# Performance work log

Measured on AMD Instinct MI355X. Metric: run time of the kernel, lower is better.

The kernel has to match this reference:

```python
import jax, jax.numpy as jnp
import numpy as np

B, T, W, D = 2, 64, 32, 512
H = 8                      # n_heads
N = 64                     # d_state
EXPAND = 2
DIN = EXPAND * D           # 1024 d_inner
R = -(-D // 16)            # dt_rank = ceil(d_model/16) = 32
K = 4                      # d_conv (mamba default)


def setup_inputs():
    key = jax.random.key(0)
    ks = jax.random.split(key, 20)
    s = 0.02
    inp = {
        'x': jax.random.normal(ks[0], (B, T, W, D), jnp.float32),
        'wq': jax.random.normal(ks[1], (D, D), jnp.float32) * s,
        'bq': jnp.zeros((D,), jnp.float32),
        'wk': jax.random.normal(ks[2], (D, D), jnp.float32) * s,
        'bk': jnp.zeros((D,), jnp.float32),
        'wv': jax.random.normal(ks[3], (D, D), jnp.float32) * s,
        'bv': jnp.zeros((D,), jnp.float32),
        'wo': jax.random.normal(ks[4], (D, D), jnp.float32) * s,
        'bo': jnp.zeros((D,), jnp.float32),
        'in_proj_w': jax.random.normal(ks[5], (2 * DIN, D), jnp.float32) * s,
        'conv_w': jax.random.normal(ks[6], (DIN, 1, K), jnp.float32) * 0.2,
        'conv_b': jnp.zeros((DIN,), jnp.float32),
        'x_proj_w': jax.random.normal(ks[7], (R + 2 * N, DIN), jnp.float32) * s,
        'dt_proj_w': jax.random.normal(ks[8], (DIN, R), jnp.float32) * 0.1,
        'dt_proj_b': jnp.full((DIN,), -4.6, jnp.float32),  # ~softplus^-1(0.01)
        'A_log': jnp.log(jnp.broadcast_to(jnp.arange(1, N + 1, dtype=jnp.float32), (DIN, N))),
        'D_param': jnp.ones((DIN,), jnp.float32),
        'out_proj_w': jax.random.normal(ks[9], (D, DIN), jnp.float32) * s,
        'ln_w': jnp.ones((D,), jnp.float32),
        'ln_b': jnp.zeros((D,), jnp.float32),
    }
    return inp


def _attention(xf, wq, bq, wk, bk, wv, bv, wo, bo):
    b, L, d = xf.shape
    e = d // H
    q = (xf @ wq.T + bq).reshape(b, L, H, e)
    k = (xf @ wk.T + bk).reshape(b, L, H, e)
    v = (xf @ wv.T + bv).reshape(b, L, H, e)
    scale = 1.0 / jnp.sqrt(jnp.float32(e))
    scores = jnp.einsum('blhe,bshe->bhls', q, k) * scale
    causal = jnp.tril(jnp.ones((L, L), bool))
    scores = jnp.where(causal, scores, jnp.finfo(scores.dtype).min)
    attn = jax.nn.softmax(scores, axis=-1)  # dropout off (eval mode)
    out = jnp.einsum('bhls,bshe->blhe', attn, v).reshape(b, L, d)
    return out @ wo.T + bo


def _mamba(xf, in_proj_w, conv_w, conv_b, x_proj_w, dt_proj_w, dt_proj_b,
           A_log, D_param, out_proj_w):
    b, L, d = xf.shape
    xz = xf @ in_proj_w.T                 # (B,L,2*DIN)
    x_in, z = jnp.split(xz, 2, axis=-1)
    # causal depthwise conv1d over L
    xc = jnp.transpose(x_in, (0, 2, 1))   # (B,DIN,L)
    xc = jax.lax.conv_general_dilated(
        xc, conv_w, window_strides=(1,), padding=[(K - 1, 0)],
        feature_group_count=DIN, dimension_numbers=('NCH', 'OIH', 'NCH'))
    xc = xc + conv_b[None, :, None]
    u = jax.nn.silu(jnp.transpose(xc, (0, 2, 1)))   # (B,L,DIN)
    dbc = u @ x_proj_w.T                             # (B,L,R+2N)
    dt, Bm, Cm = dbc[..., :R], dbc[..., R:R + N], dbc[..., R + N:]
    dt = jax.nn.softplus(dt @ dt_proj_w.T + dt_proj_b)  # (B,L,DIN)
    A = -jnp.exp(A_log)                                 # (DIN,N)

    def step(h, t):
        dt_t, B_t, C_t, u_t = t  # (b,DIN),(b,N),(b,N),(b,DIN)
        dA = jnp.exp(dt_t[..., None] * A)                       # (b,DIN,N)
        h = dA * h + (dt_t * u_t)[..., None] * B_t[:, None, :]  # (b,DIN,N)
        y = jnp.einsum('bdn,bn->bd', h, C_t)
        return h, y

    h0 = jnp.zeros((b, DIN, N), xf.dtype)
    xs = (jnp.swapaxes(dt, 0, 1), jnp.swapaxes(Bm, 0, 1),
          jnp.swapaxes(Cm, 0, 1), jnp.swapaxes(u, 0, 1))
    _, ys = jax.lax.scan(step, h0, xs)
    y = jnp.swapaxes(ys, 0, 1) + u * D_param   # (B,L,DIN)
    y = y * jax.nn.silu(z)
    return y @ out_proj_w.T


def reference(x, wq, bq, wk, bk, wv, bv, wo, bo, in_proj_w, conv_w, conv_b,
              x_proj_w, dt_proj_w, dt_proj_b, A_log, D_param, out_proj_w,
              ln_w, ln_b):
    b, t, w, d = x.shape
    L = t * w
    xf = x.reshape(b, L, d)
    x_attn = _attention(xf, wq, bq, wk, bk, wv, bv, wo, bo).reshape(b, t, w, d)
    x_mamba = _mamba(xf, in_proj_w, conv_w, conv_b, x_proj_w, dt_proj_w,
                     dt_proj_b, A_log, D_param, out_proj_w).reshape(b, t, w, d)
    h = x + x_attn + x_mamba
    mu = jnp.mean(h, axis=-1, keepdims=True)
    var = jnp.mean(jnp.square(h - mu), axis=-1, keepdims=True)
    return (h - mu) * jax.lax.rsqrt(var + 1e-5) * ln_w + ln_b
```

## Files before the change

### kernel.cpp

```cpp
#include <hip/hip_runtime.h>

typedef __attribute__((ext_vector_type(4))) float f32x4;
typedef __attribute__((ext_vector_type(8))) short short8;
typedef __attribute__((ext_vector_type(2))) unsigned uint2e;

#define DEV static __device__ __forceinline__

DEV ushort f2b(float f) {
  union { float f; unsigned u; } v; v.f = f;
  unsigned r = v.u + 0x7FFF + ((v.u >> 16) & 1);
  return (ushort)(r >> 16);
}
DEV unsigned pack_bf2(float lo, float hi) {
  return (unsigned)f2b(lo) | ((unsigned)f2b(hi) << 16);
}
DEV float bflo(unsigned p) { return __uint_as_float(p << 16); }
DEV float bfhi(unsigned p) { return __uint_as_float(p & 0xFFFF0000u); }
DEV float b2f(ushort u) { return __uint_as_float((unsigned)u << 16); }

DEV float fexp2(float x) { float r; asm("v_exp_f32 %0, %1" : "=v"(r) : "v"(x)); return r; }

DEV float xor32_add_lo(float s) {
  uint2e r = __builtin_amdgcn_permlane32_swap(__float_as_uint(s), __float_as_uint(s), false, false);
  return s + __uint_as_float(r.x);
}

DEV void gl_lds16(const ushort* g, ushort* l) {
  __builtin_amdgcn_global_load_lds(
      (const __attribute__((address_space(1))) unsigned int*)g,
      (__attribute__((address_space(3))) unsigned int*)l, 16, 0, 0);
}

#define QP(x, ctrl) __int_as_float(__builtin_amdgcn_update_dpp(0, __float_as_int(x), (ctrl), 0xf, 0xf, false))
#define SWZ(x, off) __int_as_float(__builtin_amdgcn_ds_swizzle(__float_as_int(x), (off)))
#define DPP_ADD(x, ctrl, rmask) \
  ((x) + __int_as_float(__builtin_amdgcn_update_dpp(0, __float_as_int(x), (ctrl), (rmask), 0xf, false)))

#define LOG2E 1.44269504f

#define BB    2
#define LL    2048
#define DD    512
#define HH    8
#define EE    64
#define DIN   1024
#define NS    64
#define RR    32
#define BL    4096
#define NCH   16
#define TC    128
#define NC    1536
#define NQ    3584
#define XOFF  1536
#define ZOFF  2560
#define MFMA(a,b,c) __builtin_amdgcn_mfma_f32_16x16x32_bf16((a),(b),(c),0,0,0)

struct CvtJobs {
  const float* src[7];
  ushort*      dst[7];
  int          n[7];
};

__global__ __launch_bounds__(256) void cvt_multi(CvtJobs j) {
  int job = blockIdx.y;
  const float* s = j.src[job];
  ushort* d = j.dst[job];
  int n = j.n[job];
  for (int i = blockIdx.x * 256 + threadIdx.x; i < n; i += gridDim.x * 256)
    d[i] = f2b(s[i]);
}

__global__ __launch_bounds__(256) void pack_wcomb(
    const float* __restrict__ wo, const float* __restrict__ opw,
    const float* __restrict__ bq, const float* __restrict__ bk,
    const float* __restrict__ bv, ushort* __restrict__ wc,
    float* __restrict__ bqi)
{
  int i = blockIdx.x * 256 + threadIdx.x;
  if (i < NQ)
    bqi[i] = (i < DD) ? bq[i] : (i < 2 * DD) ? bk[i - DD] : (i < NC) ? bv[i - 2 * DD] : 0.f;
  if (i >= DD * NC) return;
  int n = i / NC, c = i - n * NC;
  float v = (c < DD) ? wo[n * DD + c] : opw[n * DIN + (c - DD)];
  wc[i] = f2b(v);
}

__global__ __launch_bounds__(256) void gemm_bt(
    const ushort* __restrict__ A, const ushort* __restrict__ W,
    const float* __restrict__ bias, float* __restrict__ outF,
    ushort* __restrict__ outB, int M, int N, int K, int act)
{
  __shared__ ushort As[64 * 32];
  __shared__ ushort Ws[64 * 32];
  int m0 = blockIdx.y * 64, n0 = blockIdx.x * 64;
  int tid = threadIdx.x, l = tid & 63, w = tid >> 6;
  int wm = (w >> 1) * 32, wn = (w & 1) * 32;
  int lr = l & 15, kl = (l >> 4) * 8;
  int srow = w * 16 + (l >> 2), scol = (l & 3) * 8;
  const ushort* gA = A + (size_t)(m0 + srow) * K + scol;
  const ushort* gW = W + (size_t)(n0 + srow) * K + scol;
  ushort* lA = As + w * 512;
  ushort* lW = Ws + w * 512;
  f32x4 acc[2][2] = {};

  for (int k0 = 0; k0 < K; k0 += 32) {
    __syncthreads();
    gl_lds16(gA, lA);
    gl_lds16(gW, lW);
    __syncthreads();
    short8 a0 = *(const short8*)&As[(wm + lr) * 32 + kl];
    short8 a1 = *(const short8*)&As[(wm + 16 + lr) * 32 + kl];
    short8 b0 = *(const short8*)&Ws[(wn + lr) * 32 + kl];
    short8 b1 = *(const short8*)&Ws[(wn + 16 + lr) * 32 + kl];
    acc[0][0] = MFMA(a0, b0, acc[0][0]);
    acc[0][1] = MFMA(a0, b1, acc[0][1]);
    acc[1][0] = MFMA(a1, b0, acc[1][0]);
    acc[1][1] = MFMA(a1, b1, acc[1][1]);
    gA += 32; gW += 32;
  }

  #pragma unroll
  for (int mi = 0; mi < 2; mi++)
    #pragma unroll
    for (int ni = 0; ni < 2; ni++) {
      int rbase = m0 + wm + mi * 16 + ((l >> 4) << 2);
      int col = n0 + wn + ni * 16 + lr;
      float bval = bias ? bias[col] : 0.f;
      #pragma unroll
      for (int r = 0; r < 4; r++) {
        float v = acc[mi][ni][r] + bval;
        if (act == 1) v = (v > 20.f) ? v : log1pf(__expf(v));
        size_t o = (size_t)(rbase + r) * N + col;
        if (outF) outF[o] = v;
        if (outB) outB[o] = f2b(v);
      }
    }
}

__global__ __launch_bounds__(256) void gemm128(
    const ushort* __restrict__ A, const ushort* __restrict__ W,
    const float* __restrict__ bias, float* __restrict__ outF,
    ushort* __restrict__ outB, int M, int N, int K)
{
  __shared__ ushort As[128 * 32];
  __shared__ ushort Ws[128 * 32];
  int tid = threadIdx.x, l = tid & 63, w = tid >> 6;
  int m0 = blockIdx.y * 128, n0 = blockIdx.x * 128;
  int wm = (w >> 1) * 64, wn = (w & 1) * 64;
  int lr = l & 15, kl = (l >> 4) * 8;
  f32x4 acc[4][4] = {};

  int srow = w * 32 + (l >> 2), scol = (l & 3) * 8;
  const ushort* gA0 = A + (size_t)(m0 + srow) * K + scol;
  const ushort* gA1 = gA0 + (size_t)16 * K;
  const ushort* gW0 = W + (size_t)(n0 + srow) * K + scol;
  const ushort* gW1 = gW0 + (size_t)16 * K;
  ushort* lA0 = As + w * 1024;
  ushort* lA1 = As + w * 1024 + 512;
  ushort* lW0 = Ws + w * 1024;
  ushort* lW1 = Ws + w * 1024 + 512;

  for (int k0 = 0; k0 < K; k0 += 32) {
    __syncthreads();
    gl_lds16(gA0, lA0);
    gl_lds16(gA1, lA1);
    gl_lds16(gW0, lW0);
    gl_lds16(gW1, lW1);
    __syncthreads();
    short8 af[4], bf[4];
    #pragma unroll
    for (int mi = 0; mi < 4; mi++) af[mi] = *(const short8*)&As[(wm + mi * 16 + lr) * 32 + kl];
    #pragma unroll
    for (int ni = 0; ni < 4; ni++) bf[ni] = *(const short8*)&Ws[(wn + ni * 16 + lr) * 32 + kl];
    #pragma unroll
    for (int mi = 0; mi < 4; mi++)
      #pragma unroll
      for (int ni = 0; ni < 4; ni++)
        acc[mi][ni] = MFMA(af[mi], bf[ni], acc[mi][ni]);
    gA0 += 32; gA1 += 32; gW0 += 32; gW1 += 32;
  }

  #pragma unroll
  for (int mi = 0; mi < 4; mi++)
    #pragma unroll
    for (int ni = 0; ni < 4; ni++) {
      int rbase = m0 + wm + mi * 16 + ((l >> 4) << 2);
      int col = n0 + wn + ni * 16 + lr;
      float bval = bias ? bias[col] : 0.f;
      #pragma unroll
      for (int r = 0; r < 4; r++) {
        float v = acc[mi][ni][r] + bval;
        size_t o = (size_t)(rbase + r) * N + col;
        if (outF) outF[o] = v;
        if (outB) outB[o] = f2b(v);
      }
    }
}

__global__ __launch_bounds__(256) void attn_xproj(
    const ushort* __restrict__ qkv, ushort* __restrict__ comb,
    const ushort* __restrict__ ub, const ushort* __restrict__ xpw,
    float* __restrict__ dbc)
{
  __shared__ ushort smem[4 * 64 * 72];
  int id = blockIdx.x;
  int tid = threadIdx.x, l = tid & 63, w = tid >> 6;

  if (id < 512) {
    typedef ushort row72[72];
    row72* Qs = (row72*)smem;
    row72* Ks = Qs + 64;
    row72* Vt = Ks + 64;
    row72* Ps = Vt + 64;
    int qt = 31 - (id & 31), h = (id >> 5) & 7, b = id >> 8;
    int w16 = w * 16, lr = l & 15, kl = (l >> 4) * 8;

    for (int i = tid; i < 512; i += 256) {
      int row = i >> 3, c8 = (i & 7) * 8;
      *(uint4*)&Qs[row][c8] =
          *(const uint4*)&qkv[((size_t)(b * LL + qt * 64 + row)) * NQ + h * EE + c8];
    }
    __syncthreads();

    float l_r[4] = {0.f, 0.f, 0.f, 0.f};
    f32x4 oacc[4] = {};
    const float SSC = 0.125f * LOG2E;

    for (int kv = 0; kv <= qt; kv++) {
      for (int i = tid; i < 512; i += 256) {
        int s = i >> 3, c8 = (i & 7) * 8;
        size_t rb = ((size_t)(b * LL + kv * 64 + s)) * NQ + h * EE + c8;
        *(uint4*)&Ks[s][c8] = *(const uint4*)&qkv[rb + DD];
        uint4 vv = *(const uint4*)&qkv[rb + 2 * DD];
        const ushort* pv = (const ushort*)&vv;
        #pragma unroll
        for (int jj = 0; jj < 8; jj++) Vt[c8 + jj][s] = pv[jj];
      }
      __syncthreads();

      f32x4 sacc[4] = {};
      #pragma unroll
      for (int kk = 0; kk < 2; kk++) {
        short8 aq = *(const short8*)&Qs[w16 + lr][kk * 32 + kl];
        #pragma unroll
        for (int nt = 0; nt < 4; nt++) {
          short8 bk8 = *(const short8*)&Ks[nt * 16 + lr][kk * 32 + kl];
          sacc[nt] = MFMA(aq, bk8, sacc[nt]);
        }
      }

      bool diag = (kv == qt);
      #pragma unroll
      for (int r = 0; r < 4; r++) {
        int rloc = w16 + ((l >> 4) << 2) + r;
        float rs = 0.f;
        #pragma unroll
        for (int nt = 0; nt < 4; nt++) {
          float v = sacc[nt][r] * SSC;
          if (diag && (nt * 16 + lr) > rloc) v = -1e30f;
          float p = fexp2(v);
          rs += p;
          Ps[rloc][nt * 16 + lr] = f2b(p);
        }
        rs += QP(rs, 0xB1);
        rs += QP(rs, 0x4E);
        rs += SWZ(rs, 0x101F);
        rs += SWZ(rs, 0x201F);
        l_r[r] += rs;
      }

      #pragma unroll
      for (int kk = 0; kk < 2; kk++) {
        short8 ap = *(const short8*)&Ps[w16 + lr][kk * 32 + kl];
        #pragma unroll
        for (int nt = 0; nt < 4; nt++) {
          short8 bv8 = *(const short8*)&Vt[nt * 16 + lr][kk * 32 + kl];
          oacc[nt] = MFMA(ap, bv8, oacc[nt]);
        }
      }
      __syncthreads();
    }

    #pragma unroll
    for (int nt = 0; nt < 4; nt++)
      #pragma unroll
      for (int r = 0; r < 4; r++) {
        int row = qt * 64 + w16 + ((l >> 4) << 2) + r;
        float v = oacc[nt][r] / l_r[r];
        comb[((size_t)(b * LL + row)) * NC + h * EE + nt * 16 + lr] = f2b(v);
      }
  } else {
    typedef ushort row40[40];
    row40* As = (row40*)smem;
    row40* Ws = As + 64;
    int rid = id - 512;
    int n0 = (rid % 3) * 64, m0 = (rid / 3) * 64;
    int wm = (w >> 1) * 32, wn = (w & 1) * 32;
    int lr = l & 15, kl = (l >> 4) * 8;
    int srow = tid >> 2, sk = (tid & 3) * 8;
    f32x4 acc[2][2] = {};

    for (int k0 = 0; k0 < DIN; k0 += 32) {
      uint4 av = *(const uint4*)&ub[(size_t)(m0 + srow) * DIN + k0 + sk];
      uint4 wv;
      if (n0 + srow < 160) wv = *(const uint4*)&xpw[(size_t)(n0 + srow) * DIN + k0 + sk];
      else { wv.x = 0; wv.y = 0; wv.z = 0; wv.w = 0; }
      *(uint4*)&As[srow][sk] = av;
      *(uint4*)&Ws[srow][sk] = wv;
      __syncthreads();
      short8 a0 = *(const short8*)&As[wm + lr][kl];
      short8 a1 = *(const short8*)&As[wm + 16 + lr][kl];
      short8 b0 = *(const short8*)&Ws[wn + lr][kl];
      short8 b1 = *(const short8*)&Ws[wn + 16 + lr][kl];
      acc[0][0] = MFMA(a0, b0, acc[0][0]);
      acc[0][1] = MFMA(a0, b1, acc[0][1]);
      acc[1][0] = MFMA(a1, b0, acc[1][0]);
      acc[1][1] = MFMA(a1, b1, acc[1][1]);
      __syncthreads();
    }

    #pragma unroll
    for (int mi = 0; mi < 2; mi++)
      #pragma unroll
      for (int ni = 0; ni < 2; ni++) {
        int rbase = m0 + wm + mi * 16 + ((l >> 4) << 2);
        int col = n0 + wn + ni * 16 + lr;
        if (col < 160) {
          #pragma unroll
          for (int r = 0; r < 4; r++)
            dbc[(size_t)(rbase + r) * 160 + col] = acc[mi][ni][r];
        }
      }
  }
}

__global__ __launch_bounds__(256) void conv_silu(
    const ushort* __restrict__ xz, const float* __restrict__ cw,
    const float* __restrict__ cb, ushort* __restrict__ ub)
{
  int i = blockIdx.x * 256 + threadIdx.x;
  int d = i & (DIN - 1);
  int r = i >> 10;
  int t0 = (r & (LL / 8 - 1)) * 8;
  int b = r >> 8;
  float c0 = cw[d * 4], c1 = cw[d * 4 + 1], c2 = cw[d * 4 + 2], c3 = cw[d * 4 + 3];
  float bias = cb[d];
  float xw[11];
  #pragma unroll
  for (int j = 0; j < 3; j++) {
    int tt = t0 - 3 + j;
    xw[j] = (tt >= 0) ? b2f(xz[((size_t)(b * LL + tt)) * NQ + XOFF + d]) : 0.f;
  }
  #pragma unroll
  for (int j = 0; j < 8; j++)
    xw[3 + j] = b2f(xz[((size_t)(b * LL + t0 + j)) * NQ + XOFF + d]);
  size_t obase = (size_t)(b * LL + t0) * DIN + d;
  #pragma unroll
  for (int j = 0; j < 8; j++) {
    float s = bias + xw[j] * c0 + xw[j + 1] * c1 + xw[j + 2] * c2 + xw[j + 3] * c3;
    ub[obase + (size_t)j * DIN] = f2b(s / (1.f + __expf(-s)));
  }
}

__global__ __launch_bounds__(256) void dt_bc(
    const float* __restrict__ dbc, const ushort* __restrict__ dtw,
    const float* __restrict__ dtb, const float* __restrict__ dpar,
    const ushort* __restrict__ ub, const ushort* __restrict__ xz,
    unsigned* __restrict__ dtu_p, unsigned* __restrict__ sg_p,
    unsigned* __restrict__ bbp, float4* __restrict__ bcp4)
{
  __shared__ ushort As[64][40];
  __shared__ ushort Ws[64][40];
  __shared__ unsigned s_a[64][65];
  __shared__ unsigned s_b[64][65];
  int id = blockIdx.x;
  int tid = threadIdx.x;
  if (id < 1024) {
    int m0 = (id >> 4) * 64, n0 = (id & 15) * 64;
    int b = m0 >> 11, t0g = m0 & (LL - 1);
    int l = tid & 63, w = tid >> 6;
    int wm = (w >> 1) * 32, wn = (w & 1) * 32;
    int lr = l & 15, kl = (l >> 4) * 8;
    int srow = tid >> 2, sk = (tid & 3) * 8;

    const float* ar = dbc + (size_t)(m0 + srow) * 160 + sk;
    short8 av;
    #pragma unroll
    for (int j = 0; j < 8; j++) ((ushort*)&av)[j] = f2b(ar[j]);
    *(short8*)&As[srow][sk] = av;
    *(uint4*)&Ws[srow][sk] = *(const uint4*)&dtw[(size_t)(n0 + srow) * RR + sk];
    __syncthreads();

    f32x4 acc[2][2] = {};
    short8 a0 = *(const short8*)&As[wm + lr][kl];
    short8 a1 = *(const short8*)&As[wm + 16 + lr][kl];
    short8 b0 = *(const short8*)&Ws[wn + lr][kl];
    short8 b1 = *(const short8*)&Ws[wn + 16 + lr][kl];
    acc[0][0] = MFMA(a0, b0, acc[0][0]);
    acc[0][1] = MFMA(a0, b1, acc[0][1]);
    acc[1][0] = MFMA(a1, b0, acc[1][0]);
    acc[1][1] = MFMA(a1, b1, acc[1][1]);

    #pragma unroll
    for (int mi = 0; mi < 2; mi++)
      #pragma unroll
      for (int ni = 0; ni < 2; ni++) {
        int rl = wm + mi * 16 + ((l >> 4) << 2);
        int cl = wn + ni * 16 + lr;
        float bval = dtb[n0 + cl];
        #pragma unroll
        for (int r = 0; r < 4; r++) {
          float v = acc[mi][ni][r] + bval;
          v = (v > 20.f) ? v : log1pf(__expf(v));
          s_a[rl + r][cl] = __float_as_uint(v);
        }
      }
    __syncthreads();

    {
      int c = tid & 63, r4 = tid >> 6;
      float Dv = dpar[n0 + c];
      #pragma unroll
      for (int k = 0; k < 16; k++) {
        int r = k * 4 + r4;
        float dtv = __uint_as_float(s_a[r][c]);
        float uv  = b2f(ub[(size_t)(m0 + r) * DIN + n0 + c]);
        float zz  = b2f(xz[(size_t)(m0 + r) * NQ + ZOFF + n0 + c]);
        float g = zz / (1.f + __expf(-zz));
        s_a[r][c] = pack_bf2(dtv, dtv * uv);
        s_b[r][c] = pack_bf2(g, uv * Dv * g);
      }
    }
    __syncthreads();

    {
      int dl = tid >> 2, q = tid & 3;
      unsigned vd[16], vs[16];
      #pragma unroll
      for (int j = 0; j < 16; j++) {
        vd[j] = s_a[q * 16 + j][dl];
        vs[j] = s_b[q * 16 + j][dl];
      }
      size_t obase = ((size_t)(b * DIN + n0 + dl)) * LL + t0g + q * 16;
      #pragma unroll
      for (int jj = 0; jj < 4; jj++) {
        *(uint4*)&dtu_p[obase + jj * 4] = *(uint4*)&vd[jj * 4];
        *(uint4*)&sg_p [obase + jj * 4] = *(uint4*)&vs[jj * 4];
      }
    }
  } else {
    int i = (id - 1024) * 256 + tid;
    int n = i & 63, tp = (i >> 6) & 1023, b = i >> 16;
    size_t r0 = ((size_t)(b * LL + 2 * tp)) * 160;
    float B0 = dbc[r0 + 32 + n],  C0 = dbc[r0 + 96 + n];
    float B1 = dbc[r0 + 192 + n], C1 = dbc[r0 + 256 + n];
    bbp[i] = pack_bf2(B0, B1);
    bcp4[i] = make_float4(B0, C0, B1, C1);
  }
}

__global__ __launch_bounds__(256) void scan_p1c(
    const unsigned* __restrict__ dtu_p, const unsigned* __restrict__ bbp,
    const float* __restrict__ alog, float* __restrict__ carry)
{
  __shared__ float ldsE[4][TC][2];
  __shared__ float hfL[NCH][NS];
  __shared__ float apL[NCH][NS];
  int tid = threadIdx.x, w = tid >> 6, l = tid & 63;
  int bid = blockIdx.x;
  int d = bid & (DIN - 1);
  int b = bid >> 10;
  float An2 = -__expf(alog[d * NS + l]) * LOG2E;

  for (int k = 0; k < 4; k++) {
    int cc = w * 4 + k;
    size_t pbase = ((size_t)(b * DIN + d)) * LL + cc * TC;
    unsigned p0 = dtu_p[pbase + l];
    unsigned p1 = dtu_p[pbase + 64 + l];
    float s0 = bflo(p0), s1 = bflo(p1);
    s0 = DPP_ADD(s0, 0x111, 0xf); s0 = DPP_ADD(s0, 0x112, 0xf);
    s0 = DPP_ADD(s0, 0x114, 0xf); s0 = DPP_ADD(s0, 0x118, 0xf);
    s0 = DPP_ADD(s0, 0x142, 0xa); s0 = DPP_ADD(s0, 0x143, 0xc);
    s1 = DPP_ADD(s1, 0x111, 0xf); s1 = DPP_ADD(s1, 0x112, 0xf);
    s1 = DPP_ADD(s1, 0x114, 0xf); s1 = DPP_ADD(s1, 0x118, 0xf);
    s1 = DPP_ADD(s1, 0x142, 0xa); s1 = DPP_ADD(s1, 0x143, 0xc);
    float T0 = __uint_as_float(__builtin_amdgcn_readlane(__float_as_uint(s0), 63));
    float T  = T0 + __uint_as_float(__builtin_amdgcn_readlane(__float_as_uint(s1), 63));
    ldsE[w][l][0]      = T - s0;
    ldsE[w][l][1]      = bfhi(p0);
    ldsE[w][64 + l][0] = (T - T0) - s1;
    ldsE[w][64 + l][1] = bfhi(p1);

    const unsigned* bq = bbp + ((size_t)(b * 1024 + cc * 64) * 64 + l);
    float h0 = 0.f, h1 = 0.f;
    for (int g = 0; g < 16; g++) {
      unsigned bv[4];
      #pragma unroll
      for (int kk = 0; kk < 4; kk++) bv[kk] = bq[kk * 64];
      const float* gb = &ldsE[w][g * 8][0];
      #pragma unroll
      for (int j = 0; j < 8; j++) {
        float2 dd = *(const float2*)(gb + j * 2);
        float Bv = (j & 1) ? bfhi(bv[j >> 1]) : bflo(bv[j >> 1]);
        float a = fexp2(dd.x * An2);
        if (j & 1) h1 += a * (dd.y * Bv);
        else       h0 += a * (dd.y * Bv);
      }
      bq += 256;
    }
    hfL[cc][l] = h0 + h1;
    apL[cc][l] = fexp2(T * An2);
  }
  __syncthreads();

  float cur = 0.f, myc[4];
  #pragma unroll
  for (int cc = 0; cc < NCH; cc++) {
    if ((cc >> 2) == w) myc[cc & 3] = cur;
    cur = apL[cc][l] * cur + hfL[cc][l];
  }
  size_t cbase = ((size_t)((b << 10) + d) * NCH) * 64 + l;
  #pragma unroll
  for (int k = 0; k < 4; k++)
    carry[cbase + (size_t)(w * 4 + k) * 64] = myc[k];
}

__global__ __launch_bounds__(256) void scan_phase3(
    const unsigned* __restrict__ dtu_p, const unsigned* __restrict__ sg_p,
    const float4* __restrict__ bcp4, const float* __restrict__ alog,
    const float* __restrict__ carry, ushort* __restrict__ ymt)
{
  __shared__ float lds[4][TC][4];
  __shared__ ushort yt[4][TC];
  int tid = threadIdx.x, w = tid >> 6, l = tid & 63;
  int wid = blockIdx.x * 4 + w;
  int d = wid & (DIN - 1);
  int c = (wid >> 10) & (NCH - 1);
  int b = wid >> 14;
  float An2 = -__expf(alog[d * NS + l]) * LOG2E;

  size_t pbase = ((size_t)(b * DIN + d)) * LL + c * TC;
  #pragma unroll
  for (int q = 0; q < 2; q++) {
    unsigned pd = dtu_p[pbase + q * 64 + l];
    unsigned pg = sg_p [pbase + q * 64 + l];
    lds[w][q * 64 + l][0] = bflo(pd);
    lds[w][q * 64 + l][1] = bfhi(pd);
    lds[w][q * 64 + l][2] = bflo(pg);
    lds[w][q * 64 + l][3] = bfhi(pg);
  }
  __syncthreads();

  float h = carry[(((size_t)((b << 10) + d) * NCH) + c) * 64 + l];
  const float4* bq = bcp4 + ((size_t)(b * 1024 + c * 64) * 64 + l);
  bool s1f = l & 1, s2f = l & 2, s4f = l & 4;
  bool wl = l < 8;

  for (int g = 0; g < 16; g++) {
    float4 bcs[4];
    bcs[0] = bq[0]; bcs[1] = bq[64]; bcs[2] = bq[128]; bcs[3] = bq[192];
    const float* gb = &lds[w][g * 8][0];
    float p[8];
    #pragma unroll
    for (int j = 0; j < 8; j++) {
      float2 dd = *(const float2*)(gb + j * 4);
      float Bv = (j & 1) ? bcs[j >> 1].z : bcs[j >> 1].x;
      float Cv = (j & 1) ? bcs[j >> 1].w : bcs[j >> 1].y;
      float a = fexp2(dd.x * An2);
      h = a * h + dd.y * Bv;
      p[j] = h * Cv;
    }
    #pragma unroll
    for (int j = 0; j < 8; j++) p[j] += QP(p[j], 0xB1);
    float q0 = s1f ? p[1] : p[0];
    float q1 = s1f ? p[3] : p[2];
    float q2 = s1f ? p[5] : p[4];
    float q3 = s1f ? p[7] : p[6];
    q0 += QP(q0, 0x4E); q1 += QP(q1, 0x4E);
    q2 += QP(q2, 0x4E); q3 += QP(q3, 0x4E);
    float r0 = s2f ? q1 : q0;
    float r1 = s2f ? q3 : q2;
    r0 += SWZ(r0, 0x101F); r1 += SWZ(r1, 0x101F);
    float s = s4f ? r1 : r0;
    s += QP(s, 0x128);
    s += SWZ(s, 0x401F);
    s = xor32_add_lo(s);

    float2 sgv = *(const float2*)(&lds[w][g * 8 + (l & 7)][2]);
    if (wl) yt[w][g * 8 + l] = f2b(s * sgv.x + sgv.y);
    bq += 256;
  }
  __syncthreads();
  unsigned vv = *(const unsigned*)&yt[w][2 * l];
  ((unsigned*)(ymt + pbase))[l] = vv;
}

__global__ __launch_bounds__(256) void transpose_ym(
    const ushort* __restrict__ ymt, ushort* __restrict__ comb)
{
  __shared__ ushort tile[64][72];
  int tid = threadIdx.x;
  int bx = blockIdx.x;
  int by = blockIdx.y;
  int b  = blockIdx.z;
  int r = tid >> 2, c16 = (tid & 3) * 16;
  const ushort* src = ymt + ((size_t)(b * DIN + bx * 64 + r)) * LL + by * 64 + c16;
  *(uint4*)&tile[r][c16]     = *(const uint4*)src;
  *(uint4*)&tile[r][c16 + 8] = *(const uint4*)(src + 8);
  __syncthreads();
  ushort tmp[16];
  #pragma unroll
  for (int j = 0; j < 16; j++) tmp[j] = tile[c16 + j][r];
  ushort* dst = comb + ((size_t)(b * LL + by * 64 + r)) * NC + DD + bx * 64 + c16;
  *(uint4*)dst       = *(uint4*)&tmp[0];
  *(uint4*)(dst + 8) = *(uint4*)&tmp[8];
}

__global__ __launch_bounds__(256) void residual_ln(
    const float* __restrict__ x, const float* __restrict__ so,
    const float* __restrict__ lw, const float* __restrict__ lb,
    float* __restrict__ out)
{
  int row = blockIdx.x * 4 + (threadIdx.x >> 6);
  int l = threadIdx.x & 63;
  size_t base = (size_t)row * DD;
  float h[8];
  float s = 0.f, s2 = 0.f;
  #pragma unroll
  for (int half = 0; half < 2; half++) {
    int c = half * 256 + l * 4;
    float4 xv = *(const float4*)(x + base + c);
    float4 sv = *(const float4*)(so + base + c);
    float* hp = h + half * 4;
    hp[0] = xv.x + sv.x;
    hp[1] = xv.y + sv.y;
    hp[2] = xv.z + sv.z;
    hp[3] = xv.w + sv.w;
    #pragma unroll
    for (int j = 0; j < 4; j++) { s += hp[j]; s2 += hp[j] * hp[j]; }
  }
  #pragma unroll
  for (int o = 1; o < 64; o <<= 1) { s += __shfl_xor(s, o); s2 += __shfl_xor(s2, o); }
  float mean = s * (1.f / DD);
  float var = s2 * (1.f / DD) - mean * mean;
  float rs = rsqrtf(var + 1e-5f);
  #pragma unroll
  for (int half = 0; half < 2; half++) {
    int c = half * 256 + l * 4;
    float4 ov;
    ov.x = (h[half*4+0] - mean) * rs * lw[c+0] + lb[c+0];
    ov.y = (h[half*4+1] - mean) * rs * lw[c+1] + lb[c+1];
    ov.z = (h[half*4+2] - mean) * rs * lw[c+2] + lb[c+2];
    ov.w = (h[half*4+3] - mean) * rs * lw[c+3] + lb[c+3];
    *(float4*)(out + base + c) = ov;
  }
}

extern "C" void kernel_launch(void* const* d_in, const int* in_sizes, int n_in,
                              void* d_out, int out_size, void* d_ws, size_t ws_size,
                              hipStream_t stream) {
  const float* x    = (const float*)d_in[0];
  const float* wq   = (const float*)d_in[1];
  const float* bq   = (const float*)d_in[2];
  const float* wk   = (const float*)d_in[3];
  const float* bk   = (const float*)d_in[4];
  const float* wv   = (const float*)d_in[5];
  const float* bv   = (const float*)d_in[6];
  const float* wo   = (const float*)d_in[7];
  const float* bo   = (const float*)d_in[8];
  const float* inw  = (const float*)d_in[9];
  const float* cw   = (const float*)d_in[10];
  const float* cb   = (const float*)d_in[11];
  const float* xpw  = (const float*)d_in[12];
  const float* dtw  = (const float*)d_in[13];
  const float* dtb  = (const float*)d_in[14];
  const float* alog = (const float*)d_in[15];
  const float* dpar = (const float*)d_in[16];
  const float* opw  = (const float*)d_in[17];
  const float* lnw  = (const float*)d_in[18];
  const float* lnb  = (const float*)d_in[19];

  char* ws = (char*)d_ws;
  size_t off = 0;
  auto alloc = [&](size_t bytes) -> void* {
    void* p = ws + off;
    off += (bytes + 255) & ~(size_t)255;
    return p;
  };

  const size_t BLD = (size_t)BL * DD;
  const size_t BLDIN = (size_t)BL * DIN;

  ushort* xf_b   = (ushort*)alloc(BLD * 2);
  ushort* wqi_b  = (ushort*)alloc((size_t)NQ * DD * 2);
  float*  bqi    = (float*)alloc(NQ * 4);
  ushort* xpw_b  = (ushort*)alloc(160 * DIN * 2);
  ushort* dtw_b  = (ushort*)alloc(DIN * RR * 2);
  ushort* wcomb_b= (ushort*)alloc((size_t)DD * NC * 2);
  ushort* qkvxz_b= (ushort*)alloc((size_t)BL * NQ * 2);
  ushort* comb_a = (ushort*)alloc((size_t)BL * NC * 2);
  float*  sum_o  = (float*)alloc(BLD * 4);
  ushort* u_b    = (ushort*)alloc(BLDIN * 2);
  float*  dbc    = (float*)alloc((size_t)BL * 160 * 4);
  ushort* ymt_b  = (ushort*)alloc(BLDIN * 2);
  unsigned* bbp  = (unsigned*)alloc((size_t)BB * (LL / 2) * NS * 4);
  float4* bcp4   = (float4*)alloc((size_t)BB * (LL / 2) * NS * sizeof(float4));
  unsigned* dtu_p = (unsigned*)alloc(BLDIN * 4);
  unsigned* sg_p  = (unsigned*)alloc(BLDIN * 4);
  const size_t SCN = (size_t)BB * DIN * NCH * 64;
  float* carry_s = (float*)alloc(SCN * 4);

  CvtJobs cj;
  cj.src[0] = x;    cj.dst[0] = xf_b;                cj.n[0] = (int)BLD;
  cj.src[1] = wq;   cj.dst[1] = wqi_b;               cj.n[1] = DD * DD;
  cj.src[2] = wk;   cj.dst[2] = wqi_b + DD * DD;     cj.n[2] = DD * DD;
  cj.src[3] = wv;   cj.dst[3] = wqi_b + 2 * DD * DD; cj.n[3] = DD * DD;
  cj.src[4] = inw;  cj.dst[4] = wqi_b + 3 * DD * DD; cj.n[4] = 2 * DIN * DD;
  cj.src[5] = xpw;  cj.dst[5] = xpw_b;               cj.n[5] = 160 * DIN;
  cj.src[6] = dtw;  cj.dst[6] = dtw_b;               cj.n[6] = DIN * RR;
  cvt_multi<<<dim3(256, 7), 256, 0, stream>>>(cj);
  pack_wcomb<<<dim3((DD * NC + 255) / 256), 256, 0, stream>>>(wo, opw, bq, bk, bv, wcomb_b, bqi);

  gemm128<<<dim3(28, 32), 256, 0, stream>>>(xf_b, wqi_b, bqi, nullptr, qkvxz_b, BL, NQ, DD);

  conv_silu<<<dim3(2048), 256, 0, stream>>>(qkvxz_b, cw, cb, u_b);

  attn_xproj<<<dim3(704), 256, 0, stream>>>(qkvxz_b, comb_a, u_b, xpw_b, dbc);

  dt_bc<<<dim3(1536), 256, 0, stream>>>(dbc, dtw_b, dtb, dpar, u_b, qkvxz_b,
                                        dtu_p, sg_p, bbp, bcp4);

  scan_p1c<<<dim3(BB * DIN), 256, 0, stream>>>(dtu_p, bbp, alog, carry_s);
  scan_phase3<<<dim3(8192), 256, 0, stream>>>(dtu_p, sg_p, bcp4, alog, carry_s, ymt_b);
  transpose_ym<<<dim3(16, 32, BB), 256, 0, stream>>>(ymt_b, comb_a);

  gemm_bt<<<dim3(8, 64), 256, 0, stream>>>(comb_a, wcomb_b, bo, sum_o, nullptr, BL, DD, NC, 0);

  residual_ln<<<dim3(1024), 256, 0, stream>>>(x, sum_o, lnw, lnb, (float*)d_out);
}
```

Baseline: 338.2 us.

## Double-buffer K/V tiles in attention with register prefetch and MFMA priority

The attention loop now prefetches the next K/V tile from global memory into registers while the current tile's QK^T, softmax and PV run, then writes it into a second LDS buffer. This drops one barrier per iteration and hides global load latency behind compute. It also raises wave priority around the MFMA sections with s_setprio. The cost is more LDS (6 tiles instead of 4) and extra registers, which may reduce occupancy.

```diff
diff --git a/kernel.cpp b/kernel.cpp
--- a/kernel.cpp
+++ b/kernel.cpp
@@ -202,43 +202,71 @@
     const ushort* __restrict__ ub, const ushort* __restrict__ xpw,
     float* __restrict__ dbc)
 {
-  __shared__ ushort smem[4 * 64 * 72];
+  __shared__ ushort smem[6 * 64 * 72];
   int id = blockIdx.x;
   int tid = threadIdx.x, l = tid & 63, w = tid >> 6;
 
   if (id < 512) {
     typedef ushort row72[72];
-    row72* Qs = (row72*)smem;
-    row72* Ks = Qs + 64;
-    row72* Vt = Ks + 64;
-    row72* Ps = Vt + 64;
+    row72* Qs  = (row72*)smem;
+    row72* Ps  = Qs + 64;
+    row72* Kb0 = Ps + 64;
+    row72* Vb0 = Kb0 + 64;
+    row72* Kb1 = Vb0 + 64;
+    row72* Vb1 = Kb1 + 64;
     int qt = 31 - (id & 31), h = (id >> 5) & 7, b = id >> 8;
     int w16 = w * 16, lr = l & 15, kl = (l >> 4) * 8;
 
+    int s_r0 = tid >> 3, c8 = (tid & 7) * 8;
+    int s_r1 = s_r0 + 32;
+
     for (int i = tid; i < 512; i += 256) {
-      int row = i >> 3, c8 = (i & 7) * 8;
-      *(uint4*)&Qs[row][c8] =
-          *(const uint4*)&qkv[((size_t)(b * LL + qt * 64 + row)) * NQ + h * EE + c8];
+      int row = i >> 3, cc = (i & 7) * 8;
+      *(uint4*)&Qs[row][cc] =
+          *(const uint4*)&qkv[((size_t)(b * LL + qt * 64 + row)) * NQ + h * EE + cc];
+    }
+
+    uint4 kr0, kr1, vr0, vr1;
+    {
+      size_t rb0 = ((size_t)(b * LL + s_r0)) * NQ + h * EE + c8;
+      size_t rb1 = ((size_t)(b * LL + s_r1)) * NQ + h * EE + c8;
+      kr0 = *(const uint4*)&qkv[rb0 + DD];
+      vr0 = *(const uint4*)&qkv[rb0 + 2 * DD];
+      kr1 = *(const uint4*)&qkv[rb1 + DD];
+      vr1 = *(const uint4*)&qkv[rb1 + 2 * DD];
+    }
+    {
+      *(uint4*)&Kb0[s_r0][c8] = kr0;
+      *(uint4*)&Kb0[s_r1][c8] = kr1;
+      const ushort* p0 = (const ushort*)&vr0;
+      const ushort* p1 = (const ushort*)&vr1;
+      #pragma unroll
+      for (int jj = 0; jj < 8; jj++) {
+        Vb0[c8 + jj][s_r0] = p0[jj];
+        Vb0[c8 + jj][s_r1] = p1[jj];
+      }
     }
     __syncthreads();
 
     float l_r[4] = {0.f, 0.f, 0.f, 0.f};
     f32x4 oacc[4] = {};
     const float SSC = 0.125f * LOG2E;
+    int cur = 0;
 
     for (int kv = 0; kv <= qt; kv++) {
-      for (int i = tid; i < 512; i += 256) {
-        int s = i >> 3, c8 = (i & 7) * 8;
-        size_t rb = ((size_t)(b * LL + kv * 64 + s)) * NQ + h * EE + c8;
-        *(uint4*)&Ks[s][c8] = *(const uint4*)&qkv[rb + DD];
-        uint4 vv = *(const uint4*)&qkv[rb + 2 * DD];
-        const ushort* pv = (const ushort*)&vv;
-        #pragma unroll
-        for (int jj = 0; jj < 8; jj++) Vt[c8 + jj][s] = pv[jj];
-      }
-      __syncthreads();
+      if (kv < qt) {
+        size_t rb0 = ((size_t)(b * LL + (kv + 1) * 64 + s_r0)) * NQ + h * EE + c8;
+        size_t rb1 = ((size_t)(b * LL + (kv + 1) * 64 + s_r1)) * NQ + h * EE + c8;
+        kr0 = *(const uint4*)&qkv[rb0 + DD];
+        vr0 = *(const uint4*)&qkv[rb0 + 2 * DD];
+        kr1 = *(const uint4*)&qkv[rb1 + DD];
+        vr1 = *(const uint4*)&qkv[rb1 + 2 * DD];
+      }
+      row72* Ks = cur ? Kb1 : Kb0;
+      row72* Vt = cur ? Vb1 : Vb0;
 
       f32x4 sacc[4] = {};
+      __builtin_amdgcn_s_setprio(1);
       #pragma unroll
       for (int kk = 0; kk < 2; kk++) {
         short8 aq = *(const short8*)&Qs[w16 + lr][kk * 32 + kl];
@@ -248,6 +276,7 @@
           sacc[nt] = MFMA(aq, bk8, sacc[nt]);
         }
       }
+      __builtin_amdgcn_s_setprio(0);
 
       bool diag = (kv == qt);
       #pragma unroll
@@ -269,6 +298,7 @@
         l_r[r] += rs;
       }
 
+      __builtin_amdgcn_s_setprio(1);
       #pragma unroll
       for (int kk = 0; kk < 2; kk++) {
         short8 ap = *(const short8*)&Ps[w16 + lr][kk * 32 + kl];
@@ -278,7 +308,23 @@
           oacc[nt] = MFMA(ap, bv8, oacc[nt]);
         }
       }
+      __builtin_amdgcn_s_setprio(0);
+
+      if (kv < qt) {
+        row72* Kn = cur ? Kb0 : Kb1;
+        row72* Vn = cur ? Vb0 : Vb1;
+        *(uint4*)&Kn[s_r0][c8] = kr0;
+        *(uint4*)&Kn[s_r1][c8] = kr1;
+        const ushort* p0 = (const ushort*)&vr0;
+        const ushort* p1 = (const ushort*)&vr1;
+        #pragma unroll
+        for (int jj = 0; jj < 8; jj++) {
+          Vn[c8 + jj][s_r0] = p0[jj];
+          Vn[c8 + jj][s_r1] = p1[jj];
+        }
+      }
       __syncthreads();
+      cur ^= 1;
     }
 
     #pragma unroll
```

Measured after the change: 334.0 us. Within noise of the previous version (-1.2%).
